# Kernel optimization log

Measured on AMD Instinct MI355X. Metric: run time of the kernel, lower is better.

Reference implementation:

```python
import jax, jax.numpy as jnp
import numpy as np

H = 16
INPUT_DIM = 1024
FEATURE_DIM = 1024
HEAD_DIM = FEATURE_DIM // H


def setup_inputs() -> dict:
    key = jax.random.key(0)
    ks = jax.random.split(key, 12)
    B, S = 4, 2048
    s = 1.0 / np.sqrt(INPUT_DIM)
    inp = {
        "data": jax.random.normal(ks[0], (B, S, INPUT_DIM), dtype=jnp.float32),
        "context": jax.random.normal(ks[1], (B, S, INPUT_DIM), dtype=jnp.float32),
        "wq": jax.random.normal(ks[2], (INPUT_DIM, FEATURE_DIM), dtype=jnp.float32) * s,
        "bq": jnp.zeros((FEATURE_DIM,), dtype=jnp.float32),
        "wk": jax.random.normal(ks[3], (INPUT_DIM, FEATURE_DIM), dtype=jnp.float32) * s,
        "bk": jnp.zeros((FEATURE_DIM,), dtype=jnp.float32),
        "wv": jax.random.normal(ks[4], (INPUT_DIM, FEATURE_DIM), dtype=jnp.float32) * s,
        "bv": jnp.zeros((FEATURE_DIM,), dtype=jnp.float32),
        "wo": jax.random.normal(ks[5], (FEATURE_DIM, INPUT_DIM), dtype=jnp.float32) * s,
        "bo": jnp.zeros((INPUT_DIM,), dtype=jnp.float32),
    }
    return inp


def reference(data, context, wq, bq, wk, bk, wv, bv, wo, bo):
    B, S1, _ = data.shape
    S2 = context.shape[1]
    # QKV projections -> (B, H, S, head_dim)
    q = (data @ wq + bq).reshape(B, S1, H, HEAD_DIM).transpose(0, 2, 1, 3)
    k = (context @ wk + bk).reshape(B, S2, H, HEAD_DIM).transpose(0, 2, 1, 3)
    v = (context @ wv + bv).reshape(B, S2, H, HEAD_DIM).transpose(0, 2, 1, 3)
    scale = 1.0 / np.sqrt(HEAD_DIM).astype(np.float32)
    scores = jnp.einsum("bhqd,bhkd->bhqk", q, k) * scale  # (B,H,S1,S2)
    # causal mask (is_causal=True, S1>1): row >= col
    causal = jnp.arange(S1)[:, None] >= jnp.arange(S2)[None, :]
    scores = jnp.where(causal, scores, -jnp.inf)
    probs = jax.nn.softmax(scores, axis=-1)
    z = jnp.einsum("bhqk,bhkd->bhqd", probs, v)  # (B,H,S1,head_dim)
    z = z.transpose(0, 2, 1, 3).reshape(B, S1, FEATURE_DIM)
    return z @ wo + bo
```

## Files before the change

kernel.cpp:

```cpp
#include <hip/hip_runtime.h>
#include <hip/hip_bf16.h>
#include <math.h>

typedef short  short8  __attribute__((ext_vector_type(8)));
typedef short  short4_ __attribute__((ext_vector_type(4)));
typedef float  f32x4   __attribute__((ext_vector_type(4)));

__device__ __forceinline__ unsigned short f2bf(float f) {
  unsigned int u = __float_as_uint(f);
  u += 0x7fffu + ((u >> 16) & 1u);
  return (unsigned short)(u >> 16);
}

__device__ __forceinline__ float fexp2(float x) {
  float r;
  asm("v_exp_f32 %0, %1" : "=v"(r) : "v"(x));
  return r;
}

__device__ __forceinline__ void load_lds16(const void* g, void* l) {
  __builtin_amdgcn_global_load_lds(
      (const __attribute__((address_space(1))) unsigned int*)g,
      (__attribute__((address_space(3))) unsigned int*)l, 16, 0, 0);
}

__device__ __forceinline__ void store_out(float* p, float v) { *p = v; }
__device__ __forceinline__ void store_out(unsigned short* p, float v) { *p = f2bf(v); }

__global__ __launch_bounds__(256) void k_prep(
    const float* __restrict__ data, const float* __restrict__ context,
    unsigned short* __restrict__ Xd, unsigned short* __restrict__ Xc,
    const float* __restrict__ wq, const float* __restrict__ wk,
    const float* __restrict__ wv, const float* __restrict__ wo,
    unsigned short* __restrict__ WqT, unsigned short* __restrict__ WkT,
    unsigned short* __restrict__ WvT, unsigned short* __restrict__ WoT)
{
  const int bid = blockIdx.x;
  if (bid < 8192) {
    const float* in = (bid < 4096) ? data : context;
    unsigned short* out = (bid < 4096) ? Xd : Xc;
    int i = ((bid & 4095) * 256 + threadIdx.x) * 8;
    const float4* p = (const float4*)(in + i);
    float4 a = p[0], b = p[1];
    union { short8 v; unsigned short s[8]; } o;
    o.s[0] = f2bf(a.x); o.s[1] = f2bf(a.y); o.s[2] = f2bf(a.z); o.s[3] = f2bf(a.w);
    o.s[4] = f2bf(b.x); o.s[5] = f2bf(b.y); o.s[6] = f2bf(b.z); o.s[7] = f2bf(b.w);
    *(short8*)(out + i) = o.v;
    return;
  }
  __shared__ float tile[64][65];
  const int wsel = (bid - 8192) >> 8;
  const int sub  = (bid - 8192) & 255;
  const float* in = (wsel == 0) ? wq : (wsel == 1) ? wk : (wsel == 2) ? wv : wo;
  unsigned short* out = (wsel == 0) ? WqT : (wsel == 1) ? WkT : (wsel == 2) ? WvT : WoT;
  const int k0 = (sub >> 4) * 64, n0 = (sub & 15) * 64;
  const int t = threadIdx.x;
  const int tr = t >> 6, tc = t & 63;
  #pragma unroll
  for (int i = 0; i < 16; i++) {
    int r = i * 4 + tr;
    tile[r][tc] = in[(size_t)(k0 + r) * 1024 + n0 + tc];
  }
  __syncthreads();
  #pragma unroll
  for (int i = 0; i < 16; i++) {
    int r = i * 4 + tr;
    out[(size_t)(n0 + r) * 1024 + k0 + tc] = f2bf(tile[tc][r]);
  }
}

template <typename OutT>
__device__ __forceinline__ void gemm_body(
    const unsigned short* __restrict__ A, const unsigned short* __restrict__ Bt,
    const float* __restrict__ bias, OutT* __restrict__ C,
    int N, int m0, int n0, bool bias_row, float oscale,
    unsigned short* Als, unsigned short* Bls)
{
  const int K = 1024;
  const int t = threadIdx.x, lane = t & 63, w = t >> 6;
  const int wm = w >> 1, wn = w & 1;
  const int l4 = lane >> 4, l15 = lane & 15;

  f32x4 acc[4][4];
  #pragma unroll
  for (int i = 0; i < 4; i++)
    #pragma unroll
    for (int j = 0; j < 4; j++) acc[i][j] = (f32x4){0.f, 0.f, 0.f, 0.f};

  #define GSTAGE(bb, kk)                                                          \
    do {                                                                          \
      _Pragma("unroll")                                                           \
      for (int i = 0; i < 4; i++) {                                               \
        int chunk = w * 256 + i * 64 + lane;                                      \
        int row = chunk >> 3, slot = chunk & 7;                                   \
        int ss = slot ^ (row & 7);                                                \
        load_lds16(A  + (size_t)(m0 + row) * K + (kk) * 64 + ss * 8,              \
                   &Als[(bb) * 8192 + chunk * 8]);                                \
        load_lds16(Bt + (size_t)(n0 + row) * K + (kk) * 64 + ss * 8,              \
                   &Bls[(bb) * 8192 + chunk * 8]);                                \
      }                                                                           \
    } while (0)

  GSTAGE(0, 0);
  __syncthreads();

  const int nk = K >> 6;
  for (int kk = 0; kk < nk; kk++) {
    const int bb = kk & 1;
    if (kk + 1 < nk) GSTAGE(bb ^ 1, kk + 1);
    const unsigned short* Ab = &Als[bb * 8192];
    const unsigned short* Bb = &Bls[bb * 8192];
    #pragma unroll
    for (int ks = 0; ks < 2; ks++) {
      short8 af[4], bf[4];
      #pragma unroll
      for (int m = 0; m < 4; m++) {
        int row = wm * 64 + m * 16 + l15;
        int sl = (ks * 4 + l4) ^ (row & 7);
        af[m] = *(const short8*)&Ab[row * 64 + sl * 8];
      }
      #pragma unroll
      for (int n = 0; n < 4; n++) {
        int row = wn * 64 + n * 16 + l15;
        int sl = (ks * 4 + l4) ^ (row & 7);
        bf[n] = *(const short8*)&Bb[row * 64 + sl * 8];
      }
      #pragma unroll
      for (int m = 0; m < 4; m++)
        #pragma unroll
        for (int n = 0; n < 4; n++)
          acc[m][n] = __builtin_amdgcn_mfma_f32_16x16x32_bf16(af[m], bf[n], acc[m][n], 0, 0, 0);
    }
    __syncthreads();
  }
  #undef GSTAGE

  #pragma unroll
  for (int m = 0; m < 4; m++)
    #pragma unroll
    for (int r = 0; r < 4; r++) {
      int row = m0 + wm * 64 + m * 16 + l4 * 4 + r;
      #pragma unroll
      for (int n = 0; n < 4; n++) {
        int col = n0 + wn * 64 + n * 16 + l15;
        float v = (acc[m][n][r] + (bias_row ? bias[row] : bias[col])) * oscale;
        store_out(&C[(size_t)row * N + col], v);
      }
    }
}

__global__ __launch_bounds__(256) void k_gemm3(
    const unsigned short* __restrict__ Xd, const unsigned short* __restrict__ Xc,
    const unsigned short* __restrict__ WqT, const unsigned short* __restrict__ WkT,
    const unsigned short* __restrict__ WvT,
    const float* __restrict__ bq, const float* __restrict__ bk, const float* __restrict__ bv,
    unsigned short* __restrict__ Qm, unsigned short* __restrict__ Km,
    unsigned short* __restrict__ Vt, float SC)
{
  __shared__ unsigned short Als[2 * 128 * 64];
  __shared__ unsigned short Bls[2 * 128 * 64];
  const int which = blockIdx.x >> 9;
  const int sub = blockIdx.x & 511;
  const int id2 = (sub & 7) * 64 + (sub >> 3);

  if (which == 0) {
    gemm_body(Xd, WqT, bq, Qm, 1024, (id2 >> 3) * 128, (id2 & 7) * 128, false, SC, Als, Bls);
  } else if (which == 1) {
    gemm_body(Xc, WkT, bk, Km, 1024, (id2 >> 3) * 128, (id2 & 7) * 128, false, 1.0f, Als, Bls);
  } else {
    gemm_body(WvT, Xc, bv, Vt, 8192, (id2 >> 6) * 128, (id2 & 63) * 128, true, 1.0f, Als, Bls);
  }
}

__global__ __launch_bounds__(256) void k_gemm_out(
    const unsigned short* __restrict__ A, const unsigned short* __restrict__ Bt,
    const float* __restrict__ bias, float* __restrict__ C)
{
  __shared__ unsigned short Als[2 * 128 * 64];
  __shared__ unsigned short Bls[2 * 128 * 64];
  const int cpx = 64;
  const int id2 = (blockIdx.x & 7) * cpx + (blockIdx.x >> 3);
  gemm_body(A, Bt, bias, C, 1024, (id2 >> 3) * 128, (id2 & 7) * 128, false, 1.0f, Als, Bls);
}

__global__ __launch_bounds__(256, 4) void k_attn(
    const unsigned short* __restrict__ Q,
    const unsigned short* __restrict__ Km,
    const unsigned short* __restrict__ Vt,
    unsigned short* __restrict__ Z)
{
  __shared__ __align__(16) unsigned short Kls[2][64 * 64];
  __shared__ __align__(16) unsigned short Vls[2][64 * 64];
  const int t = threadIdx.x, lane = t & 63, w = t >> 6;
  const int l4 = lane >> 4, l15 = lane & 15;
  const int qt = 15 - (int)(blockIdx.x >> 6);
  const int bh = blockIdx.x & 63;
  const int h = bh & 15, b = bh >> 4;
  const int jend = 2 * qt + 1;
  const int wrow = qt * 128 + w * 32;
  const int jdiag = wrow >> 6;

  const int xr = l15 & 7;
  const int base0 = l15 * 64 + ((l4)     ^ xr) * 8;
  const int base1 = l15 * 64 + ((4 + l4) ^ xr) * 8;
  const unsigned short* Kp0 = &Kls[0][0] + base0;
  const unsigned short* Kp1 = &Kls[0][0] + base1;
  const char* Vc0; const char* Vc1; const char* Vc2; const char* Vc3;
  {
    const char* Vbase = (const char*)&Vls[0][0] + l15 * 128 + ((l4 & 1) << 3);
    const int a = l4 >> 1;
    Vc0 = Vbase + (((0 | a) ^ xr) << 4);
    Vc1 = Vbase + (((2 | a) ^ xr) << 4);
    Vc2 = Vbase + (((4 | a) ^ xr) << 4);
    Vc3 = Vbase + (((6 | a) ^ xr) << 4);
  }

  const int c0 = t, c1 = t + 256;
  const int r0 = c0 >> 3, s0 = (c0 & 7) ^ (r0 & 7);
  const int r1 = c1 >> 3, s1 = (c1 & 7) ^ (r1 & 7);
  const size_t kg0 = ((size_t)b * 2048 + r0) * 1024 + h * 64 + s0 * 8;
  const size_t kg1 = ((size_t)b * 2048 + r1) * 1024 + h * 64 + s1 * 8;
  const size_t vg0 = ((size_t)h * 64 + r0) * 8192 + (size_t)b * 2048 + s0 * 8;
  const size_t vg1 = ((size_t)h * 64 + r1) * 8192 + (size_t)b * 2048 + s1 * 8;

  #define STAGE(bb, j)                                                \
    do {                                                              \
      load_lds16(Km + kg0 + (size_t)(j) * 65536, &Kls[bb][c0 * 8]);   \
      load_lds16(Km + kg1 + (size_t)(j) * 65536, &Kls[bb][c1 * 8]);   \
      load_lds16(Vt + vg0 + (size_t)(j) * 64,    &Vls[bb][c0 * 8]);   \
      load_lds16(Vt + vg1 + (size_t)(j) * 64,    &Vls[bb][c1 * 8]);   \
    } while (0)

  short8 qfA[2], qfB[2];
  {
    size_t qrA = ((size_t)b * 2048 + wrow + l15) * 1024 + h * 64;
    size_t qrB = qrA + 16 * 1024;
    #pragma unroll
    for (int ks = 0; ks < 2; ks++) {
      qfA[ks] = *(const short8*)&Q[qrA + ks * 32 + l4 * 8];
      qfB[ks] = *(const short8*)&Q[qrB + ks * 32 + l4 * 8];
    }
  }
  short8 ones;
  #pragma unroll
  for (int i = 0; i < 8; i++) ones[i] = (short)0x3F80;
  const f32x4 zf = (f32x4){0.f, 0.f, 0.f, 0.f};

  f32x4 oaccA[4], oaccB[4], lsumA, lsumB;
  #pragma unroll
  for (int n = 0; n < 4; n++) {
    oaccA[n] = zf;
    oaccB[n] = zf;
  }
  lsumA = zf;
  lsumB = zf;

  STAGE(0, 0);
  asm volatile("s_waitcnt vmcnt(0)" ::: "memory");
  __syncthreads();

  auto SM = [&](f32x4 (&s)[4], int qbase, int j, bool diag, short8& pf0, short8& pf1) {
    if (diag) {
      const int q = qbase + l15;
      const int kb = j * 64 + l4 * 4;
      #pragma unroll
      for (int n = 0; n < 4; n++)
        #pragma unroll
        for (int r = 0; r < 4; r++)
          if (kb + n * 16 + r > q) s[n][r] = -__builtin_inff();
    }
    float p[4][4];
    #pragma unroll
    for (int n = 0; n < 4; n++)
      #pragma unroll
      for (int r = 0; r < 4; r++) p[n][r] = fexp2(s[n][r]);
    unsigned int lo0, hi0, lo1, hi1, lo2, hi2, lo3, hi3;
    asm("v_cvt_pk_bf16_f32 %0, %1, %2" : "=v"(lo0) : "v"(p[0][0]), "v"(p[0][1]));
    asm("v_cvt_pk_bf16_f32 %0, %1, %2" : "=v"(hi0) : "v"(p[0][2]), "v"(p[0][3]));
    asm("v_cvt_pk_bf16_f32 %0, %1, %2" : "=v"(lo1) : "v"(p[1][0]), "v"(p[1][1]));
    asm("v_cvt_pk_bf16_f32 %0, %1, %2" : "=v"(hi1) : "v"(p[1][2]), "v"(p[1][3]));
    asm("v_cvt_pk_bf16_f32 %0, %1, %2" : "=v"(lo2) : "v"(p[2][0]), "v"(p[2][1]));
    asm("v_cvt_pk_bf16_f32 %0, %1, %2" : "=v"(hi2) : "v"(p[2][2]), "v"(p[2][3]));
    asm("v_cvt_pk_bf16_f32 %0, %1, %2" : "=v"(lo3) : "v"(p[3][0]), "v"(p[3][1]));
    asm("v_cvt_pk_bf16_f32 %0, %1, %2" : "=v"(hi3) : "v"(p[3][2]), "v"(p[3][3]));
    union { unsigned int d[4]; short8 s8; } u0, u1;
    u0.d[0] = lo0; u0.d[1] = hi0; u0.d[2] = lo1; u0.d[3] = hi1;
    u1.d[0] = lo2; u1.d[1] = hi2; u1.d[2] = lo3; u1.d[3] = hi3;
    pf0 = u0.s8;
    pf1 = u1.s8;
  };

  int buf = 0;
  for (int j = 0; j <= jend; ++j) {
    if (j < jend) STAGE(buf ^ 1, j + 1);

    if (j * 64 <= wrow) {
      const unsigned short* Kb0 = Kp0 + buf * 4096;
      const unsigned short* Kb1 = Kp1 + buf * 4096;
      const int bo = buf * 8192;

      f32x4 sA[4], sB[4];
      __builtin_amdgcn_s_setprio(1);
      #pragma unroll
      for (int n = 0; n < 4; n++) {
        short8 kf = *(const short8*)(Kb0 + n * 1024);
        sA[n] = __builtin_amdgcn_mfma_f32_16x16x32_bf16(kf, qfA[0], zf, 0, 0, 0);
        sB[n] = __builtin_amdgcn_mfma_f32_16x16x32_bf16(kf, qfB[0], zf, 0, 0, 0);
      }
      #pragma unroll
      for (int n = 0; n < 4; n++) {
        short8 kf = *(const short8*)(Kb1 + n * 1024);
        sA[n] = __builtin_amdgcn_mfma_f32_16x16x32_bf16(kf, qfA[1], sA[n], 0, 0, 0);
        sB[n] = __builtin_amdgcn_mfma_f32_16x16x32_bf16(kf, qfB[1], sB[n], 0, 0, 0);
      }
      __builtin_amdgcn_s_setprio(0);

      const bool diag = (j == jdiag);
      short8 pfA0, pfA1, pfB0, pfB1;
      SM(sA, wrow,      j, diag, pfA0, pfA1);
      SM(sB, wrow + 16, j, diag, pfB0, pfB1);

      __builtin_amdgcn_s_setprio(1);
      lsumA = __builtin_amdgcn_mfma_f32_16x16x32_bf16(pfA0, ones, lsumA, 0, 0, 0);
      lsumB = __builtin_amdgcn_mfma_f32_16x16x32_bf16(pfB0, ones, lsumB, 0, 0, 0);
      #pragma unroll
      for (int n = 0; n < 4; n++) {
        union { short4_ h[2]; short8 s8; } vv;
        vv.h[0] = *(const short4_*)(Vc0 + bo + n * 2048);
        vv.h[1] = *(const short4_*)(Vc1 + bo + n * 2048);
        oaccA[n] = __builtin_amdgcn_mfma_f32_16x16x32_bf16(pfA0, vv.s8, oaccA[n], 0, 0, 0);
        oaccB[n] = __builtin_amdgcn_mfma_f32_16x16x32_bf16(pfB0, vv.s8, oaccB[n], 0, 0, 0);
      }
      lsumA = __builtin_amdgcn_mfma_f32_16x16x32_bf16(pfA1, ones, lsumA, 0, 0, 0);
      lsumB = __builtin_amdgcn_mfma_f32_16x16x32_bf16(pfB1, ones, lsumB, 0, 0, 0);
      #pragma unroll
      for (int n = 0; n < 4; n++) {
        union { short4_ h[2]; short8 s8; } vv;
        vv.h[0] = *(const short4_*)(Vc2 + bo + n * 2048);
        vv.h[1] = *(const short4_*)(Vc3 + bo + n * 2048);
        oaccA[n] = __builtin_amdgcn_mfma_f32_16x16x32_bf16(pfA1, vv.s8, oaccA[n], 0, 0, 0);
        oaccB[n] = __builtin_amdgcn_mfma_f32_16x16x32_bf16(pfB1, vv.s8, oaccB[n], 0, 0, 0);
      }
      __builtin_amdgcn_s_setprio(0);
    }

    asm volatile("s_waitcnt vmcnt(0)" ::: "memory");
    __syncthreads();
    buf ^= 1;
  }
  #undef STAGE

  #pragma unroll
  for (int r = 0; r < 4; r++) {
    float invA = 1.f / lsumA[r];
    float invB = 1.f / lsumB[r];
    size_t rowA = (size_t)b * 2048 + wrow + l4 * 4 + r;
    size_t rowB = rowA + 16;
    #pragma unroll
    for (int n = 0; n < 4; n++) {
      Z[rowA * 1024 + h * 64 + n * 16 + l15] = f2bf(oaccA[n][r] * invA);
      Z[rowB * 1024 + h * 64 + n * 16 + l15] = f2bf(oaccB[n][r] * invB);
    }
  }
}

extern "C" void kernel_launch(void* const* d_in, const int* in_sizes, int n_in,
                              void* d_out, int out_size, void* d_ws, size_t ws_size,
                              hipStream_t stream) {
  const float* data = (const float*)d_in[0];
  const float* context = (const float*)d_in[1];
  const float* wq = (const float*)d_in[2];
  const float* bq = (const float*)d_in[3];
  const float* wk = (const float*)d_in[4];
  const float* bk = (const float*)d_in[5];
  const float* wv = (const float*)d_in[6];
  const float* bv = (const float*)d_in[7];
  const float* wo = (const float*)d_in[8];
  const float* bo = (const float*)d_in[9];
  float* out = (float*)d_out;

  char* ws = (char*)d_ws;
  const size_t SZ_X = (size_t)8192 * 1024 * 2;
  const size_t SZ_W = (size_t)1024 * 1024 * 2;
  unsigned short* Xd  = (unsigned short*)(ws);
  unsigned short* Xc  = (unsigned short*)(ws + SZ_X);
  unsigned short* WqT = (unsigned short*)(ws + 2 * SZ_X);
  unsigned short* WkT = (unsigned short*)(ws + 2 * SZ_X + SZ_W);
  unsigned short* WvT = (unsigned short*)(ws + 2 * SZ_X + 2 * SZ_W);
  unsigned short* WoT = (unsigned short*)(ws + 2 * SZ_X + 3 * SZ_W);
  unsigned short* Qm  = (unsigned short*)(ws + 2 * SZ_X + 4 * SZ_W);
  unsigned short* Km  = (unsigned short*)(ws + 3 * SZ_X + 4 * SZ_W);
  unsigned short* Vt  = (unsigned short*)(ws + 4 * SZ_X + 4 * SZ_W);
  unsigned short* Zm  = (unsigned short*)(ws + 5 * SZ_X + 4 * SZ_W);

  const float SC = 0.125f * 1.44269504f;

  k_prep<<<9216, 256, 0, stream>>>(data, context, Xd, Xc, wq, wk, wv, wo,
                                   WqT, WkT, WvT, WoT);

  k_gemm3<<<1536, 256, 0, stream>>>(Xd, Xc, WqT, WkT, WvT, bq, bk, bv, Qm, Km, Vt, SC);

  k_attn<<<1024, 256, 0, stream>>>(Qm, Km, Vt, Zm);

  k_gemm_out<<<512, 256, 0, stream>>>(Zm, WoT, bo, out);
}
```

Before: 161.5 us.

## Restructure GEMM mainloop to prefetch two stages ahead with explicit waitcnt and setprio

The GEMM main loop now issues global-to-LDS loads two k-tiles ahead instead of one. It replaces __syncthreads with explicit vmcnt/lgkmcnt waits and raw barriers. All LDS fragments for the tile are read into registers before the buffer is refilled, and the MFMA block is wrapped in s_setprio to favour the math phase. The aim is to hide more global-load latency and cut barrier stalls in the QKV and output projections. In exchange it raises register pressure by holding both k-substeps' fragments, and it relies on hand-counted vmcnt values being correct.

```diff
diff --git a/kernel.cpp b/kernel.cpp
--- a/kernel.cpp
+++ b/kernel.cpp
@@ -70,7 +70,7 @@
 }
 
 template <typename OutT>
-__device__ __forceinline__ void gemm_body(
+__device__ __forceinline__ void gemm_body_cv(
     const unsigned short* __restrict__ A, const unsigned short* __restrict__ Bt,
     const float* __restrict__ bias, OutT* __restrict__ C,
     int N, int m0, int n0, bool bias_row, float oscale,
@@ -102,36 +102,45 @@
     } while (0)
 
   GSTAGE(0, 0);
-  __syncthreads();
+  GSTAGE(1, 1);
 
   const int nk = K >> 6;
   for (int kk = 0; kk < nk; kk++) {
-    const int bb = kk & 1;
-    if (kk + 1 < nk) GSTAGE(bb ^ 1, kk + 1);
-    const unsigned short* Ab = &Als[bb * 8192];
-    const unsigned short* Bb = &Bls[bb * 8192];
+    if (kk + 1 < nk) { asm volatile("s_waitcnt vmcnt(8)" ::: "memory"); }
+    else             { asm volatile("s_waitcnt vmcnt(0)" ::: "memory"); }
+    __builtin_amdgcn_s_barrier();
+
+    const unsigned short* Ab = &Als[(kk & 1) * 8192];
+    const unsigned short* Bb = &Bls[(kk & 1) * 8192];
+    short8 af[2][4], bf[2][4];
     #pragma unroll
     for (int ks = 0; ks < 2; ks++) {
-      short8 af[4], bf[4];
       #pragma unroll
       for (int m = 0; m < 4; m++) {
         int row = wm * 64 + m * 16 + l15;
         int sl = (ks * 4 + l4) ^ (row & 7);
-        af[m] = *(const short8*)&Ab[row * 64 + sl * 8];
+        af[ks][m] = *(const short8*)&Ab[row * 64 + sl * 8];
       }
       #pragma unroll
       for (int n = 0; n < 4; n++) {
         int row = wn * 64 + n * 16 + l15;
         int sl = (ks * 4 + l4) ^ (row & 7);
-        bf[n] = *(const short8*)&Bb[row * 64 + sl * 8];
-      }
+        bf[ks][n] = *(const short8*)&Bb[row * 64 + sl * 8];
+      }
+    }
+    asm volatile("s_waitcnt lgkmcnt(0)" ::: "memory");
+    __builtin_amdgcn_s_barrier();
+    if (kk + 2 < nk) GSTAGE(kk & 1, kk + 2);
+
+    __builtin_amdgcn_s_setprio(1);
+    #pragma unroll
+    for (int ks = 0; ks < 2; ks++)
       #pragma unroll
       for (int m = 0; m < 4; m++)
         #pragma unroll
         for (int n = 0; n < 4; n++)
-          acc[m][n] = __builtin_amdgcn_mfma_f32_16x16x32_bf16(af[m], bf[n], acc[m][n], 0, 0, 0);
-    }
-    __syncthreads();
+          acc[m][n] = __builtin_amdgcn_mfma_f32_16x16x32_bf16(af[ks][m], bf[ks][n], acc[m][n], 0, 0, 0);
+    __builtin_amdgcn_s_setprio(0);
   }
   #undef GSTAGE
 
@@ -157,18 +166,18 @@
     unsigned short* __restrict__ Qm, unsigned short* __restrict__ Km,
     unsigned short* __restrict__ Vt, float SC)
 {
-  __shared__ unsigned short Als[2 * 128 * 64];
-  __shared__ unsigned short Bls[2 * 128 * 64];
+  __shared__ unsigned short Als[2 * 8192];
+  __shared__ unsigned short Bls[2 * 8192];
   const int which = blockIdx.x >> 9;
   const int sub = blockIdx.x & 511;
   const int id2 = (sub & 7) * 64 + (sub >> 3);
 
   if (which == 0) {
-    gemm_body(Xd, WqT, bq, Qm, 1024, (id2 >> 3) * 128, (id2 & 7) * 128, false, SC, Als, Bls);
+    gemm_body_cv(Xd, WqT, bq, Qm, 1024, (id2 >> 3) * 128, (id2 & 7) * 128, false, SC, Als, Bls);
   } else if (which == 1) {
-    gemm_body(Xc, WkT, bk, Km, 1024, (id2 >> 3) * 128, (id2 & 7) * 128, false, 1.0f, Als, Bls);
+    gemm_body_cv(Xc, WkT, bk, Km, 1024, (id2 >> 3) * 128, (id2 & 7) * 128, false, 1.0f, Als, Bls);
   } else {
-    gemm_body(WvT, Xc, bv, Vt, 8192, (id2 >> 6) * 128, (id2 & 63) * 128, true, 1.0f, Als, Bls);
+    gemm_body_cv(WvT, Xc, bv, Vt, 8192, (id2 >> 6) * 128, (id2 & 63) * 128, true, 1.0f, Als, Bls);
   }
 }
 
@@ -176,11 +185,11 @@
     const unsigned short* __restrict__ A, const unsigned short* __restrict__ Bt,
     const float* __restrict__ bias, float* __restrict__ C)
 {
-  __shared__ unsigned short Als[2 * 128 * 64];
-  __shared__ unsigned short Bls[2 * 128 * 64];
+  __shared__ unsigned short Als[2 * 8192];
+  __shared__ unsigned short Bls[2 * 8192];
   const int cpx = 64;
   const int id2 = (blockIdx.x & 7) * cpx + (blockIdx.x >> 3);
-  gemm_body(A, Bt, bias, C, 1024, (id2 >> 3) * 128, (id2 & 7) * 128, false, 1.0f, Als, Bls);
+  gemm_body_cv(A, Bt, bias, C, 1024, (id2 >> 3) * 128, (id2 & 7) * 128, false, 1.0f, Als, Bls);
 }
 
 __global__ __launch_bounds__(256, 4) void k_attn(
```

Result: faster. 148.8 us, median of 2 (-7.9%).
